# Kernel optimization log

Measured on AMD Instinct MI355X. Metric: run time of the kernel, lower is better.

Reference implementation:

```python
import jax, jax.numpy as jnp
import numpy as np

B, T_EN, T_DE, D_EN, D_DE, UNITS = 16, 256, 256, 512, 512, 128


def setup_inputs() -> dict:
    key = jax.random.key(0)
    k1, k2, k3, k4, k5 = jax.random.split(key, 5)
    # glorot-uniform style scale for weights
    def glorot(k, shape):
        lim = np.sqrt(6.0 / (shape[0] + shape[1]))
        return jax.random.uniform(k, shape, jnp.float32, -lim, lim)
    return {
        "en_seq": jax.random.normal(k1, (B, T_EN, D_EN), jnp.float32),
        "de_seq": jax.random.normal(k2, (B, T_DE, D_DE), jnp.float32),
        "w_en": glorot(k3, (D_EN, UNITS)),
        "w_de": glorot(k4, (D_DE, UNITS)),
        "nu": glorot(k5, (UNITS, 1)),
    }


def reference(en_seq, de_seq, w_en, w_de, nu):
    # Additive (Bahdanau) time attention.
    # Original keras code builds the (de, en) cross product via K.repeat /
    # K.repeat_elements with de-major, en-minor ordering; equivalent to
    # broadcasting att_de over a new en axis and att_en over a new de axis.
    att_en = jnp.einsum("bie,eu->biu", en_seq, w_en)   # (B, T_en, U)
    att_de = jnp.einsum("bjd,du->bju", de_seq, w_de)   # (B, T_de, U)
    # co_m: (B, T_de, T_en, U) — the large broadcast intermediate
    co_m = jnp.tanh(att_de[:, :, None, :] + att_en[:, None, :, :])
    mu = jnp.einsum("bjiu,u->bji", co_m, nu[:, 0])      # (B, T_de, T_en)
    alphas = jax.nn.softmax(mu, axis=-1)                # softmax over encoder time
    sum_en = jnp.einsum("bji,bie->bje", alphas, en_seq)  # (B, T_de, D_en)
    return jnp.concatenate([de_seq, sum_en], axis=-1)    # (B, T_de, D_de + D_en)
```

## Files before the change

kernel.cpp:

```cpp
#include <hip/hip_runtime.h>
#include <hip/hip_bf16.h>

#define TANH_SCALE 2.8853900817779268f

__global__ __launch_bounds__(256, 4) void proj2_kernel(
        const float* __restrict__ en, const float* __restrict__ de,
        const float* __restrict__ w_en, const float* __restrict__ w_de,
        float* __restrict__ Een, float* __restrict__ Ede) {
    const float* X;
    const float* W;
    float* OUT;
    if (blockIdx.y == 0) { X = en; W = w_en; OUT = Een; }
    else                 { X = de; W = w_de; OUT = Ede; }

    __shared__ float w_sh[64][128];
    __shared__ float x_sh[8][64];
    const int tid  = threadIdx.x;
    const int u    = tid & 127;
    const int half = tid >> 7;
    const int row0 = blockIdx.x * 8;

    float acc[4] = {0.0f, 0.0f, 0.0f, 0.0f};

    for (int kt = 0; kt < 512; kt += 64) {
        const float4* Wg = reinterpret_cast<const float4*>(W + (size_t)kt * 128);
        float4* wsh4 = reinterpret_cast<float4*>(&w_sh[0][0]);
#pragma unroll
        for (int t = 0; t < 8; ++t) wsh4[tid + 256 * t] = Wg[tid + 256 * t];
        if (tid < 128) {
            int r = tid >> 4, kk4 = (tid & 15) * 4;
            reinterpret_cast<float4*>(&x_sh[0][0])[tid] =
                *reinterpret_cast<const float4*>(X + (size_t)(row0 + r) * 512 + kt + kk4);
        }
        __syncthreads();
#pragma unroll
        for (int kk = 0; kk < 64; kk += 4) {
            float w0 = w_sh[kk][u], w1 = w_sh[kk + 1][u];
            float w2 = w_sh[kk + 2][u], w3 = w_sh[kk + 3][u];
#pragma unroll
            for (int r = 0; r < 4; ++r) {
                float4 x4 = *reinterpret_cast<const float4*>(&x_sh[half * 4 + r][kk]);
                acc[r] = fmaf(x4.x, w0, acc[r]);
                acc[r] = fmaf(x4.y, w1, acc[r]);
                acc[r] = fmaf(x4.z, w2, acc[r]);
                acc[r] = fmaf(x4.w, w3, acc[r]);
            }
        }
        __syncthreads();
    }
#pragma unroll
    for (int r = 0; r < 4; ++r)
        OUT[(size_t)(row0 + half * 4 + r) * 128 + u] =
            __builtin_exp2f(-TANH_SCALE * acc[r]);
}

__global__ __launch_bounds__(512, 4) void fused_attn_kernel(
        const float* __restrict__ Een, const float* __restrict__ Ede,
        const float* __restrict__ nu, const float* __restrict__ en,
        const float* __restrict__ de, float* __restrict__ out) {
    const int phys = blockIdx.x;
    const int lid  = (phys & 7) * 64 + (phys >> 3);
    const int b    = lid >> 5;
    const int j0   = (lid & 31) * 8;
    const int tid  = threadIdx.x;
    const int i    = tid & 255;
    const int uh   = tid >> 8;

    __shared__ float ede_sh[8][128];
    __shared__ float nu2_sh[128];
    __shared__ float al[8][256];
    __shared__ float red[8][4];

    if (tid < 256)
        reinterpret_cast<float4*>(&ede_sh[0][0])[tid] =
            reinterpret_cast<const float4*>(Ede + ((size_t)b * 256 + j0) * 128)[tid];
    if (tid >= 256 && tid < 384) nu2_sh[tid - 256] = 2.0f * nu[tid - 256];

    {
        const float4* dsrc =
            reinterpret_cast<const float4*>(de + ((size_t)b * 256 + j0) * 512);
#pragma unroll
        for (int t = 0; t < 2; ++t) {
            int idx = tid + 512 * t;
            int j = idx >> 7, c4 = idx & 127;
            reinterpret_cast<float4*>(out + (size_t)(b * 256 + j0 + j) * 1024)[c4] =
                dsrc[idx];
        }
    }
    __syncthreads();

    float s[4] = {0.0f, 0.0f, 0.0f, 0.0f};
    const float4* e4 =
        reinterpret_cast<const float4*>(Een + ((size_t)b * 256 + i) * 128);
    for (int q = 0; q < 8; ++q) {
        float ev[16], nv[16];
#pragma unroll
        for (int t = 0; t < 4; ++t) {
            float4 a = e4[q * 4 + t];
            ev[4 * t] = a.x; ev[4 * t + 1] = a.y; ev[4 * t + 2] = a.z; ev[4 * t + 3] = a.w;
            float4 n = *reinterpret_cast<const float4*>(&nu2_sh[q * 16 + 4 * t]);
            nv[4 * t] = n.x; nv[4 * t + 1] = n.y; nv[4 * t + 2] = n.z; nv[4 * t + 3] = n.w;
        }
#pragma unroll
        for (int jl = 0; jl < 4; ++jl) {
            const int j = uh * 4 + jl;
            float dv[16];
#pragma unroll
            for (int t = 0; t < 4; ++t) {
                float4 d = *reinterpret_cast<const float4*>(&ede_sh[j][q * 16 + 4 * t]);
                dv[4 * t] = d.x; dv[4 * t + 1] = d.y; dv[4 * t + 2] = d.z; dv[4 * t + 3] = d.w;
            }
#pragma unroll
            for (int t = 0; t < 16; ++t) {
                float e = ev[t] * dv[t];
                float r = __builtin_amdgcn_rcpf(1.0f + e);
                s[jl] = fmaf(nv[t], r, s[jl]);
            }
        }
    }

    float p[4];
#pragma unroll
    for (int jl = 0; jl < 4; ++jl) p[jl] = __expf(s[jl]);
    const int lane = tid & 63;
    const int w    = (tid >> 6) & 3;
#pragma unroll
    for (int jl = 0; jl < 4; ++jl) {
        float t = p[jl];
#pragma unroll
        for (int off = 32; off >= 1; off >>= 1) t += __shfl_xor(t, off);
        if (lane == 0) red[uh * 4 + jl][w] = t;
    }
    __syncthreads();
#pragma unroll
    for (int jl = 0; jl < 4; ++jl) {
        const int j = uh * 4 + jl;
        float T = red[j][0] + red[j][1] + red[j][2] + red[j][3];
        al[j][i] = p[jl] * __builtin_amdgcn_rcpf(T);
    }
    __syncthreads();

    float acc[8];
#pragma unroll
    for (int j = 0; j < 8; ++j) acc[j] = 0.0f;
    const float* enb = en + (size_t)b * 256 * 512;
    const int c = tid;
    for (int i0 = 0; i0 < 256; i0 += 4) {
        float a[8][4];
#pragma unroll
        for (int j = 0; j < 8; ++j) {
            float4 v = *reinterpret_cast<const float4*>(&al[j][i0]);
            a[j][0] = v.x; a[j][1] = v.y; a[j][2] = v.z; a[j][3] = v.w;
        }
#pragma unroll
        for (int ii = 0; ii < 4; ++ii) {
            float e0 = enb[(size_t)(i0 + ii) * 512 + c];
#pragma unroll
            for (int j = 0; j < 8; ++j)
                acc[j] = fmaf(a[j][ii], e0, acc[j]);
        }
    }
#pragma unroll
    for (int j = 0; j < 8; ++j) {
        size_t row = (size_t)(b * 256 + j0 + j);
        out[row * 1024 + 512 + c] = acc[j];
    }
}

extern "C" void kernel_launch(void* const* d_in, const int* in_sizes, int n_in,
                              void* d_out, int out_size, void* d_ws, size_t ws_size,
                              hipStream_t stream) {
    const float* en   = (const float*)d_in[0];
    const float* de   = (const float*)d_in[1];
    const float* w_en = (const float*)d_in[2];
    const float* w_de = (const float*)d_in[3];
    const float* nu   = (const float*)d_in[4];
    float* out = (float*)d_out;

    char* ws = (char*)d_ws;
    float* Een = (float*)(ws);
    float* Ede = (float*)(ws + (size_t)4096 * 128 * 4);

    proj2_kernel<<<dim3(512, 2), 256, 0, stream>>>(en, de, w_en, w_de, Een, Ede);
    fused_attn_kernel<<<dim3(512), 512, 0, stream>>>(Een, Ede, nu, en, de, out);
}
```

Before: 163.8 us.

## Register-tile projection GEMM with prefetch and pair tanh reciprocals

Rewrites the projection kernel so each thread computes a 4x4 register tile over a 32-row block. It uses a transposed, swizzled LDS layout for X and register-staged prefetch of the next K tile, which raises FMA-to-load ratio and hides global latency. Separately, the attention score loop combines two sigmoid-style terms over a common denominator, halving the reciprocal count at the cost of extra FMAs and a precomputed nu-pair sum. The pairing changes rounding slightly and could overflow when products are large.

```diff
diff --git a/kernel.cpp b/kernel.cpp
--- a/kernel.cpp
+++ b/kernel.cpp
@@ -3,7 +3,7 @@
 
 #define TANH_SCALE 2.8853900817779268f
 
-__global__ __launch_bounds__(256, 4) void proj2_kernel(
+__global__ __launch_bounds__(256) void proj_kernel(
         const float* __restrict__ en, const float* __restrict__ de,
         const float* __restrict__ w_en, const float* __restrict__ w_de,
         float* __restrict__ Een, float* __restrict__ Ede) {
@@ -13,45 +13,97 @@
     if (blockIdx.y == 0) { X = en; W = w_en; OUT = Een; }
     else                 { X = de; W = w_de; OUT = Ede; }
 
-    __shared__ float w_sh[64][128];
-    __shared__ float x_sh[8][64];
+    __shared__ float xt[64][36];
+    __shared__ float wsh[64][128];
     const int tid  = threadIdx.x;
-    const int u    = tid & 127;
-    const int half = tid >> 7;
-    const int row0 = blockIdx.x * 8;
-
-    float acc[4] = {0.0f, 0.0f, 0.0f, 0.0f};
+    const int tr   = tid >> 5;
+    const int tc   = tid & 31;
+    const int row0 = blockIdx.x * 32;
+
+    const int xs_r  = tid >> 4;
+    const int xs_k4 = (tid & 15) * 4;
+    float4 xr[2], wr[8];
+
+    auto g_load = [&](int kt) {
+#pragma unroll
+        for (int s = 0; s < 2; ++s) {
+            int r = xs_r + 16 * s;
+            xr[s] = *reinterpret_cast<const float4*>(
+                X + (size_t)(row0 + r) * 512 + kt + xs_k4);
+        }
+#pragma unroll
+        for (int s = 0; s < 8; ++s) {
+            int idx = tid + 256 * s;
+            int k = idx >> 5, c4 = (idx & 31) * 4;
+            wr[s] = *reinterpret_cast<const float4*>(
+                W + (size_t)(kt + k) * 128 + c4);
+        }
+    };
+    auto lds_store = [&]() {
+        const int swz = ((xs_k4 >> 2) & 7) << 2;
+#pragma unroll
+        for (int s = 0; s < 2; ++s) {
+            int r = (xs_r + 16 * s) ^ swz;
+            xt[xs_k4 + 0][r] = xr[s].x;
+            xt[xs_k4 + 1][r] = xr[s].y;
+            xt[xs_k4 + 2][r] = xr[s].z;
+            xt[xs_k4 + 3][r] = xr[s].w;
+        }
+#pragma unroll
+        for (int s = 0; s < 8; ++s) {
+            int idx = tid + 256 * s;
+            int k = idx >> 5, c4 = (idx & 31) * 4;
+            *reinterpret_cast<float4*>(&wsh[k][c4]) = wr[s];
+        }
+    };
+
+    float acc[4][4] = {{0.f}};
+    g_load(0);
+    lds_store();
+    __syncthreads();
 
     for (int kt = 0; kt < 512; kt += 64) {
-        const float4* Wg = reinterpret_cast<const float4*>(W + (size_t)kt * 128);
-        float4* wsh4 = reinterpret_cast<float4*>(&w_sh[0][0]);
-#pragma unroll
-        for (int t = 0; t < 8; ++t) wsh4[tid + 256 * t] = Wg[tid + 256 * t];
-        if (tid < 128) {
-            int r = tid >> 4, kk4 = (tid & 15) * 4;
-            reinterpret_cast<float4*>(&x_sh[0][0])[tid] =
-                *reinterpret_cast<const float4*>(X + (size_t)(row0 + r) * 512 + kt + kk4);
+        const bool has_next = (kt + 64) < 512;
+        if (has_next) g_load(kt + 64);
+#pragma unroll
+        for (int k = 0; k < 64; ++k) {
+            const int col = (tr * 4) ^ (((k >> 2) & 7) << 2);
+            float4 xv = *reinterpret_cast<const float4*>(&xt[k][col]);
+            float4 wv = *reinterpret_cast<const float4*>(&wsh[k][tc * 4]);
+            acc[0][0] = fmaf(xv.x, wv.x, acc[0][0]);
+            acc[0][1] = fmaf(xv.x, wv.y, acc[0][1]);
+            acc[0][2] = fmaf(xv.x, wv.z, acc[0][2]);
+            acc[0][3] = fmaf(xv.x, wv.w, acc[0][3]);
+            acc[1][0] = fmaf(xv.y, wv.x, acc[1][0]);
+            acc[1][1] = fmaf(xv.y, wv.y, acc[1][1]);
+            acc[1][2] = fmaf(xv.y, wv.z, acc[1][2]);
+            acc[1][3] = fmaf(xv.y, wv.w, acc[1][3]);
+            acc[2][0] = fmaf(xv.z, wv.x, acc[2][0]);
+            acc[2][1] = fmaf(xv.z, wv.y, acc[2][1]);
+            acc[2][2] = fmaf(xv.z, wv.z, acc[2][2]);
+            acc[2][3] = fmaf(xv.z, wv.w, acc[2][3]);
+            acc[3][0] = fmaf(xv.w, wv.x, acc[3][0]);
+            acc[3][1] = fmaf(xv.w, wv.y, acc[3][1]);
+            acc[3][2] = fmaf(xv.w, wv.z, acc[3][2]);
+            acc[3][3] = fmaf(xv.w, wv.w, acc[3][3]);
         }
         __syncthreads();
-#pragma unroll
-        for (int kk = 0; kk < 64; kk += 4) {
-            float w0 = w_sh[kk][u], w1 = w_sh[kk + 1][u];
-            float w2 = w_sh[kk + 2][u], w3 = w_sh[kk + 3][u];
-#pragma unroll
-            for (int r = 0; r < 4; ++r) {
-                float4 x4 = *reinterpret_cast<const float4*>(&x_sh[half * 4 + r][kk]);
-                acc[r] = fmaf(x4.x, w0, acc[r]);
-                acc[r] = fmaf(x4.y, w1, acc[r]);
-                acc[r] = fmaf(x4.z, w2, acc[r]);
-                acc[r] = fmaf(x4.w, w3, acc[r]);
-            }
-        }
-        __syncthreads();
-    }
-#pragma unroll
-    for (int r = 0; r < 4; ++r)
-        OUT[(size_t)(row0 + half * 4 + r) * 128 + u] =
-            __builtin_exp2f(-TANH_SCALE * acc[r]);
+        if (has_next) {
+            lds_store();
+            __syncthreads();
+        }
+    }
+
+#pragma unroll
+    for (int r = 0; r < 4; ++r) {
+        float4 o;
+        o.x = __builtin_exp2f(-TANH_SCALE * acc[r][0]);
+        o.y = __builtin_exp2f(-TANH_SCALE * acc[r][1]);
+        o.z = __builtin_exp2f(-TANH_SCALE * acc[r][2]);
+        o.w = __builtin_exp2f(-TANH_SCALE * acc[r][3]);
+        *reinterpret_cast<float4*>(
+            OUT + (size_t)(row0 + tr * 4 + r) * 128 + tc * 4) = o;
+    }
 }
 
 __global__ __launch_bounds__(512, 4) void fused_attn_kernel(
@@ -68,6 +120,7 @@
 
     __shared__ float ede_sh[8][128];
     __shared__ float nu2_sh[128];
+    __shared__ float nusum_sh[64];
     __shared__ float al[8][256];
     __shared__ float red[8][4];
 
@@ -75,6 +128,10 @@
         reinterpret_cast<float4*>(&ede_sh[0][0])[tid] =
             reinterpret_cast<const float4*>(Ede + ((size_t)b * 256 + j0) * 128)[tid];
     if (tid >= 256 && tid < 384) nu2_sh[tid - 256] = 2.0f * nu[tid - 256];
+    if (tid >= 384 && tid < 448) {
+        int t = tid - 384;
+        nusum_sh[t] = 2.0f * (nu[2 * t] + nu[2 * t + 1]);
+    }
 
     {
         const float4* dsrc =
@@ -92,8 +149,9 @@
     float s[4] = {0.0f, 0.0f, 0.0f, 0.0f};
     const float4* e4 =
         reinterpret_cast<const float4*>(Een + ((size_t)b * 256 + i) * 128);
+#pragma unroll
     for (int q = 0; q < 8; ++q) {
-        float ev[16], nv[16];
+        float ev[16], nv[16], cs[8];
 #pragma unroll
         for (int t = 0; t < 4; ++t) {
             float4 a = e4[q * 4 + t];
@@ -102,6 +160,8 @@
             nv[4 * t] = n.x; nv[4 * t + 1] = n.y; nv[4 * t + 2] = n.z; nv[4 * t + 3] = n.w;
         }
 #pragma unroll
+        for (int t2 = 0; t2 < 8; ++t2) cs[t2] = nusum_sh[q * 8 + t2];
+#pragma unroll
         for (int jl = 0; jl < 4; ++jl) {
             const int j = uh * 4 + jl;
             float dv[16];
@@ -111,10 +171,14 @@
                 dv[4 * t] = d.x; dv[4 * t + 1] = d.y; dv[4 * t + 2] = d.z; dv[4 * t + 3] = d.w;
             }
 #pragma unroll
-            for (int t = 0; t < 16; ++t) {
-                float e = ev[t] * dv[t];
-                float r = __builtin_amdgcn_rcpf(1.0f + e);
-                s[jl] = fmaf(nv[t], r, s[jl]);
+            for (int t2 = 0; t2 < 8; ++t2) {
+                float e0 = ev[2 * t2]     * dv[2 * t2];
+                float e1 = ev[2 * t2 + 1] * dv[2 * t2 + 1];
+                float den = 1.0f + e0;
+                den = fmaf(den, e1, den);
+                float num = fmaf(nv[2 * t2], e1, cs[t2]);
+                num = fmaf(nv[2 * t2 + 1], e0, num);
+                s[jl] = fmaf(num, __builtin_amdgcn_rcpf(den), s[jl]);
             }
         }
     }
@@ -181,6 +245,6 @@
     float* Een = (float*)(ws);
     float* Ede = (float*)(ws + (size_t)4096 * 128 * 4);
 
-    proj2_kernel<<<dim3(512, 2), 256, 0, stream>>>(en, de, w_en, w_de, Een, Ede);
+    proj_kernel<<<dim3(128, 2), 256, 0, stream>>>(en, de, w_en, w_de, Een, Ede);
     fused_attn_kernel<<<dim3(512), 512, 0, stream>>>(Een, Ede, nu, en, de, out);
 }
```

Measured after the change: 607.5 us. 3.71x slower.
